# Performance work log

Measured on AMD Instinct MI355X. Metric: run time of the kernel, lower is better.

## Reference

```python
import jax
import jax.numpy as jnp
import numpy as np
from jax import lax

# D dags, L topological levels, K nodes per level, P predecessors per node,
# F = atom/hidden feature dim (104 in original), C = num classes (500)
D, L, K, P, F, C = 256, 64, 64, 8, 104, 500


def setup_inputs() -> dict:
    key = jax.random.key(0)
    ks = jax.random.split(key, 10)
    atom_feats = jax.random.normal(ks[0], (D, L, K, F), dtype=jnp.float32)
    pred_idx = jax.random.randint(ks[1], (D, L - 1, K, P), 0, K, dtype=jnp.int32)
    W1 = jax.random.normal(ks[2], (F, F), dtype=jnp.float32) * 0.1
    b1 = jnp.zeros((F,), dtype=jnp.float32)
    Wm = jax.random.normal(ks[3], (2 * F, F), dtype=jnp.float32) * 0.1
    bm = jnp.zeros((F,), dtype=jnp.float32)
    att_w = jax.random.uniform(ks[4], (F,), dtype=jnp.float32)  # torch.rand init
    dag_w = jax.random.uniform(ks[5], (F,), dtype=jnp.float32)
    Wf = jax.random.normal(ks[6], (F, C), dtype=jnp.float32) * 0.1
    bf = jnp.zeros((C,), dtype=jnp.float32)
    return {"atom_feats": atom_feats, "pred_idx": pred_idx, "W1": W1, "b1": b1,
            "Wm": Wm, "bm": bm, "att_w": att_w, "dag_w": dag_w, "Wf": Wf, "bf": bf}


def reference(atom_feats, pred_idx, W1, b1, Wm, bm, att_w, dag_w, Wf, bf):
    # Level 0: source nodes -> ReLU(NN_single_node(atom))
    out0 = jax.nn.relu(atom_feats[:, 0] @ W1 + b1)  # [D, K, F]

    def step(prev, xs):
        atoms, idx = xs  # atoms [D,K,F], idx [D,K,P]
        # gather predecessor outputs from previous topological level
        preds = jax.vmap(lambda p, i: p[i])(prev, idx)  # [D,K,P,F]
        # softmax attention over the predecessor (stack) axis, elementwise in F
        attn = jax.nn.softmax(att_w * preds, axis=2)
        agg = jnp.sum(attn * preds, axis=2)  # [D,K,F]
        # cat((aggregated, atom)) -> merge -> ReLU
        out = jax.nn.relu(jnp.concatenate([agg, atoms], axis=-1) @ Wm + bm)
        return out, None

    xs = (jnp.swapaxes(atom_feats[:, 1:], 0, 1),  # [L-1, D, K, F]
          jnp.swapaxes(pred_idx, 0, 1))           # [L-1, D, K, P]
    last, _ = lax.scan(step, out0, xs)
    # 'last' output per DAG = last node in topological order
    sink = last[:, -1]  # [D, F]
    # softmax attention over DAG axis with dag_weight, then final linear
    dag_attn = jax.nn.softmax(dag_w * sink, axis=0)
    pooled = jnp.sum(dag_attn * sink, axis=0)  # [F]
    return pooled @ Wf + bf  # [C]
```

## Files before the change

### kernel.cpp

```cpp
#include <hip/hip_runtime.h>
#include <cstddef>
#include <math.h>

#define Dn 256
#define Ln 64
#define Kn 64
#define Pn 8
#define Fn 104
#define Cn 500
#define KF 6656
#define TPB 896
#define PSTR 108
#define XROWB 512
#define NQ 1664

typedef __attribute__((ext_vector_type(8))) short bh8;
typedef __attribute__((ext_vector_type(4))) float f32x4;

__device__ __forceinline__ unsigned short f2bf_rne(float x) {
  unsigned u = __builtin_bit_cast(unsigned, x);
  u = (u + 0x7fffu + ((u >> 16) & 1u)) >> 16;
  return (unsigned short)u;
}
__device__ __forceinline__ float bf2f(unsigned short h) {
  unsigned u = ((unsigned)h) << 16;
  return __builtin_bit_cast(float, u);
}
__device__ __forceinline__ unsigned pkhi(float a, float b) {
  return __builtin_amdgcn_perm(__builtin_bit_cast(unsigned, b),
                               __builtin_bit_cast(unsigned, a), 0x07060302u);
}
__device__ __forceinline__ float hi_of(float x) {
  return __builtin_bit_cast(float, __builtin_bit_cast(unsigned, x) & 0xffff0000u);
}

__device__ __forceinline__ void stage_quad(char* XAc, char* XBc, int k, int c0,
                                           float v0, float v1, float v2, float v3) {
  uint2 hv, lv;
  hv.x = pkhi(v0, v1); hv.y = pkhi(v2, v3);
  const float r0 = v0 - hi_of(v0), r1 = v1 - hi_of(v1);
  const float r2 = v2 - hi_of(v2), r3 = v3 - hi_of(v3);
  lv.x = pkhi(r0, r1); lv.y = pkhi(r2, r3);
  const int off = k * XROWB + ((((c0 >> 3) ^ (k & 7)) << 4) | ((c0 & 7) << 1));
  *reinterpret_cast<uint2*>(XAc + off) = hv;
  *reinterpret_cast<uint2*>(XBc + off) = lv;
}

__device__ __forceinline__ void load_w_frags(const float* __restrict__ Wg, int Krows,
                                             int col, int e, bh8* Wh, bh8* Wl) {
  #pragma unroll
  for (int kt = 0; kt < 7; ++kt) {
    bh8 h, l;
    #pragma unroll
    for (int v = 0; v < 8; ++v) {
      int k = kt * 32 + e * 8 + v;
      float x = (k < Krows && col < Fn) ? Wg[k * Fn + col] : 0.f;
      unsigned short hh = f2bf_rne(x);
      unsigned short ll = f2bf_rne(x - bf2f(hh));
      h[v] = (short)hh; l[v] = (short)ll;
    }
    Wh[kt] = h; Wl[kt] = l;
  }
}

__device__ __forceinline__ void mfma_gemm(const char* XAc, const char* XBc,
                                          const bh8* Wh, const bh8* Wl,
                                          const float* bms, float* PREVs,
                                          int lane, int col, int mh,
                                          int k0, int k1) {
  const int e = lane >> 4;
  const int rb = lane & 15;
  const float bias = (col < Fn) ? bms[col] : 0.f;
  f32x4 acc[2];
  #pragma unroll
  for (int mti = 0; mti < 2; ++mti) { f32x4 b4 = {bias, bias, bias, bias}; acc[mti] = b4; }
  #pragma unroll
  for (int kt = 0; kt < 7; ++kt) {
    if (kt < k0 || kt >= k1) continue;
    #pragma unroll
    for (int mti = 0; mti < 2; ++mti) {
      const int r = (mh * 2 + mti) * 16 + rb;
      const int chunk = (kt * 4 + e) ^ (rb & 7);
      const bh8 ah = *reinterpret_cast<const bh8*>(XAc + r * XROWB + chunk * 16);
      const bh8 al = *reinterpret_cast<const bh8*>(XBc + r * XROWB + chunk * 16);
      acc[mti] = __builtin_amdgcn_mfma_f32_16x16x32_bf16(ah, Wh[kt], acc[mti], 0, 0, 0);
      acc[mti] = __builtin_amdgcn_mfma_f32_16x16x32_bf16(al, Wh[kt], acc[mti], 0, 0, 0);
      acc[mti] = __builtin_amdgcn_mfma_f32_16x16x32_bf16(ah, Wl[kt], acc[mti], 0, 0, 0);
    }
  }
  if (col < Fn) {
    #pragma unroll
    for (int mti = 0; mti < 2; ++mti) {
      #pragma unroll
      for (int j = 0; j < 4; ++j) {
        int r = (mh * 2 + mti) * 16 + e * 4 + j;
        PREVs[r * PSTR + col] = fmaxf(acc[mti][j], 0.f);
      }
    }
  }
}

__global__ __launch_bounds__(TPB) void scan_kernel(
    const float* __restrict__ af,
    const int*   __restrict__ pidx,
    const float* __restrict__ W1, const float* __restrict__ b1,
    const float* __restrict__ Wm, const float* __restrict__ bm,
    const float* __restrict__ att_w,
    float* __restrict__ sink)
{
  extern __shared__ char smem[];
  char*  XAc   = smem;
  char*  XBc   = smem + 32768;
  float* PREVs = (float*)(smem + 65536);
  float* bms   = (float*)(smem + 65536 + 27648);
  float* aws   = (float*)(smem + 65536 + 27648 + 448);
  int*   idxs  = (int*)  (smem + 65536 + 27648 + 448 + 416);

  const int t = threadIdx.x;
  const int d = blockIdx.x;
  const int lane = t & 63;
  const int wvi = t >> 6;
  const int nt = wvi % 7;
  const int mh = wvi / 7;
  const int e = lane >> 4;
  const int col = nt * 16 + (lane & 15);

  const float*  afd = af + (size_t)d * (Ln * KF);
  const float4* af4 = reinterpret_cast<const float4*>(afd);
  const int*    pid = pidx + (size_t)d * ((Ln - 1) * Kn * Pn);

  bh8 Wh[7], Wl[7];
  float4 pf4[2];
  int ir0 = 0;

  for (int i = t; i < 16384; i += TPB) reinterpret_cast<unsigned*>(XAc)[i] = 0u;
  if (t < Fn) { bms[t] = b1[t]; aws[t] = att_w[t]; }
  else if (t < 112) bms[t] = 0.f;
  load_w_frags(W1, Fn, col, e, Wh, Wl);
  #pragma unroll
  for (int j = 0; j < 2; ++j) {
    int q = t + j * TPB;
    if (q < NQ) {
      int k = q / 26, fq = (q - k * 26) << 2;
      float4 v = af4[q];
      stage_quad(XAc, XBc, k, fq, v.x, v.y, v.z, v.w);
    }
  }
  __syncthreads();

  mfma_gemm(XAc, XBc, Wh, Wl, bms, PREVs, lane, col, mh, 0, 4);
  __syncthreads();

  load_w_frags(Wm, 2 * Fn, col, e, Wh, Wl);
  if (t < Fn) bms[t] = bm[t];
  if (t < 512) idxs[t] = pid[t];
  #pragma unroll
  for (int j = 0; j < 2; ++j) {
    int q = t + j * TPB;
    if (q < NQ) pf4[j] = af4[NQ + q];
  }
  __syncthreads();

  for (int l = 1; l < Ln; ++l) {
    #pragma unroll
    for (int j = 0; j < 2; ++j) {
      int q = t + j * TPB;
      if (q < NQ) {
        int k = q / 26, fq = (q - k * 26) << 2;
        float4 v = pf4[j];
        stage_quad(XAc, XBc, k, Fn + fq, v.x, v.y, v.z, v.w);
      }
    }
    if (l < 63) {
      const float4* an = af4 + (size_t)(l + 1) * NQ;
      #pragma unroll
      for (int j = 0; j < 2; ++j) {
        int q = t + j * TPB;
        if (q < NQ) pf4[j] = an[q];
      }
      if (t < 512) ir0 = pid[(size_t)l * 512 + t];
    }
    for (int q = t; q < NQ; q += TPB) {
      int k = q / 26, fq = (q - k * 26) << 2;
      const float4 w4 = *reinterpret_cast<const float4*>(aws + fq);
      const float wa[4] = {w4.x, w4.y, w4.z, w4.w};
      const int4 ia = *reinterpret_cast<const int4*>(idxs + (k << 3));
      const int4 ib = *reinterpret_cast<const int4*>(idxs + (k << 3) + 4);
      const int ip[8] = {ia.x, ia.y, ia.z, ia.w, ib.x, ib.y, ib.z, ib.w};
      float vv[8][4];
      #pragma unroll
      for (int p = 0; p < Pn; ++p) {
        float4 v4 = *reinterpret_cast<const float4*>(PREVs + ip[p] * PSTR + fq);
        vv[p][0] = v4.x; vv[p][1] = v4.y; vv[p][2] = v4.z; vv[p][3] = v4.w;
      }
      float ag[4];
      #pragma unroll
      for (int c = 0; c < 4; ++c) {
        float vmax = fmaxf(fmaxf(fmaxf(fmaxf(fmaxf(fmaxf(fmaxf(
            vv[0][c], vv[1][c]), vv[2][c]), vv[3][c]), vv[4][c]), vv[5][c]), vv[6][c]), vv[7][c]);
        const float m = wa[c] * vmax;
        float es = 0.f, ps = 0.f;
        #pragma unroll
        for (int p = 0; p < Pn; ++p) {
          float ex = __expf(fmaf(wa[c], vv[p][c], -m));
          es += ex; ps += ex * vv[p][c];
        }
        ag[c] = ps * __builtin_amdgcn_rcpf(es);
      }
      stage_quad(XAc, XBc, k, fq, ag[0], ag[1], ag[2], ag[3]);
    }
    __syncthreads();

    mfma_gemm(XAc, XBc, Wh, Wl, bms, PREVs, lane, col, mh, 0, 7);
    if (l < 63 && t < 512) idxs[t] = ir0;
    __syncthreads();
  }

  if (t < Fn) sink[d * Fn + t] = PREVs[(Kn - 1) * PSTR + t];
}

__global__ __launch_bounds__(512) void final_kernel(
    const float* __restrict__ sink, const float* __restrict__ dag_w,
    const float* __restrict__ Wf, const float* __restrict__ bf,
    float* __restrict__ out)
{
  extern __shared__ char smem[];
  float* ss = (float*)smem;
  float* pooled = ss + Dn * Fn;
  const int t = threadIdx.x;
  for (int i = t; i < Dn * Fn; i += 512) ss[i] = sink[i];
  __syncthreads();
  if (t < Fn) {
    float wvv = dag_w[t];
    float m = -3.0e38f;
    for (int dd = 0; dd < Dn; ++dd) m = fmaxf(m, wvv * ss[dd * Fn + t]);
    float es = 0.f, ps = 0.f;
    for (int dd = 0; dd < Dn; ++dd) {
      float v = ss[dd * Fn + t];
      float ex = __expf(wvv * v - m);
      es += ex; ps += ex * v;
    }
    pooled[t] = ps / es;
  }
  __syncthreads();
  if (t < Cn) {
    float a = bf[t];
    for (int f = 0; f < Fn; ++f) a = fmaf(pooled[f], Wf[f * Cn + t], a);
    out[t] = a;
  }
}

extern "C" void kernel_launch(void* const* d_in, const int* in_sizes, int n_in,
                              void* d_out, int out_size, void* d_ws, size_t ws_size,
                              hipStream_t stream) {
  const float* af    = (const float*)d_in[0];
  const int*   pidx  = (const int*)  d_in[1];
  const float* W1    = (const float*)d_in[2];
  const float* b1    = (const float*)d_in[3];
  const float* Wm    = (const float*)d_in[4];
  const float* bm    = (const float*)d_in[5];
  const float* att_w = (const float*)d_in[6];
  const float* dag_w = (const float*)d_in[7];
  const float* Wf    = (const float*)d_in[8];
  const float* bf    = (const float*)d_in[9];
  float* out  = (float*)d_out;
  float* sink = (float*)d_ws;

  constexpr size_t SMEM1 = 96096;
  constexpr size_t SMEM2 = (size_t)(Dn * Fn + Fn) * 4;

  (void)hipFuncSetAttribute((const void*)scan_kernel,
                      hipFuncAttributeMaxDynamicSharedMemorySize, (int)SMEM1);
  (void)hipFuncSetAttribute((const void*)final_kernel,
                      hipFuncAttributeMaxDynamicSharedMemorySize, (int)SMEM2);

  scan_kernel<<<Dn, TPB, SMEM1, stream>>>(af, pidx, W1, b1, Wm, bm, att_w, sink);
  final_kernel<<<1, 512, SMEM2, stream>>>(sink, dag_w, Wf, bf, out);
}
```

Baseline: 354.8 us.

## Split merge GEMM to compute atom-feature half before aggregation

The merge GEMM is split by K-tiles. The atom-feature half (kt 4..6) now runs right after the atom features are staged, before the softmax aggregation. Its partial accumulators are parked in a new shared-memory buffer, and the aggregation half finishes the GEMM after the barrier. This shortens the serial GEMM that follows aggregation and lets MFMA work overlap with the gather phase. The cost is an extra __syncthreads per level, about 28 KB more LDS, and a store/reload of the accumulators.

```diff
diff --git a/kernel.cpp b/kernel.cpp
--- a/kernel.cpp
+++ b/kernel.cpp
@@ -63,31 +63,26 @@
   }
 }
 
-__device__ __forceinline__ void mfma_gemm(const char* XAc, const char* XBc,
-                                          const bh8* Wh, const bh8* Wl,
-                                          const float* bms, float* PREVs,
-                                          int lane, int col, int mh,
-                                          int k0, int k1) {
+__device__ __forceinline__ void mfma_kt(const char* XAc, const char* XBc,
+                                        const bh8* Wh, const bh8* Wl,
+                                        f32x4 acc[2], int kt, int lane, int mh) {
   const int e = lane >> 4;
   const int rb = lane & 15;
-  const float bias = (col < Fn) ? bms[col] : 0.f;
-  f32x4 acc[2];
   #pragma unroll
-  for (int mti = 0; mti < 2; ++mti) { f32x4 b4 = {bias, bias, bias, bias}; acc[mti] = b4; }
-  #pragma unroll
-  for (int kt = 0; kt < 7; ++kt) {
-    if (kt < k0 || kt >= k1) continue;
-    #pragma unroll
-    for (int mti = 0; mti < 2; ++mti) {
-      const int r = (mh * 2 + mti) * 16 + rb;
-      const int chunk = (kt * 4 + e) ^ (rb & 7);
-      const bh8 ah = *reinterpret_cast<const bh8*>(XAc + r * XROWB + chunk * 16);
-      const bh8 al = *reinterpret_cast<const bh8*>(XBc + r * XROWB + chunk * 16);
-      acc[mti] = __builtin_amdgcn_mfma_f32_16x16x32_bf16(ah, Wh[kt], acc[mti], 0, 0, 0);
-      acc[mti] = __builtin_amdgcn_mfma_f32_16x16x32_bf16(al, Wh[kt], acc[mti], 0, 0, 0);
-      acc[mti] = __builtin_amdgcn_mfma_f32_16x16x32_bf16(ah, Wl[kt], acc[mti], 0, 0, 0);
-    }
-  }
+  for (int mti = 0; mti < 2; ++mti) {
+    const int r = (mh * 2 + mti) * 16 + rb;
+    const int chunk = (kt * 4 + e) ^ (rb & 7);
+    const bh8 ah = *reinterpret_cast<const bh8*>(XAc + r * XROWB + chunk * 16);
+    const bh8 al = *reinterpret_cast<const bh8*>(XBc + r * XROWB + chunk * 16);
+    acc[mti] = __builtin_amdgcn_mfma_f32_16x16x32_bf16(ah, Wh[kt], acc[mti], 0, 0, 0);
+    acc[mti] = __builtin_amdgcn_mfma_f32_16x16x32_bf16(al, Wh[kt], acc[mti], 0, 0, 0);
+    acc[mti] = __builtin_amdgcn_mfma_f32_16x16x32_bf16(ah, Wl[kt], acc[mti], 0, 0, 0);
+  }
+}
+
+__device__ __forceinline__ void gemm_epilogue(f32x4 acc[2], float* PREVs,
+                                              int lane, int col, int mh) {
+  const int e = lane >> 4;
   if (col < Fn) {
     #pragma unroll
     for (int mti = 0; mti < 2; ++mti) {
@@ -115,6 +110,7 @@
   float* bms   = (float*)(smem + 65536 + 27648);
   float* aws   = (float*)(smem + 65536 + 27648 + 448);
   int*   idxs  = (int*)  (smem + 65536 + 27648 + 448 + 416);
+  float* PC    = (float*)(smem + 96096);
 
   const int t = threadIdx.x;
   const int d = blockIdx.x;
@@ -148,7 +144,15 @@
   }
   __syncthreads();
 
-  mfma_gemm(XAc, XBc, Wh, Wl, bms, PREVs, lane, col, mh, 0, 4);
+  {
+    const float bias = (col < Fn) ? bms[col] : 0.f;
+    f32x4 acc[2];
+    #pragma unroll
+    for (int mti = 0; mti < 2; ++mti) { f32x4 b4 = {bias, bias, bias, bias}; acc[mti] = b4; }
+    #pragma unroll
+    for (int kt = 0; kt < 4; ++kt) mfma_kt(XAc, XBc, Wh, Wl, acc, kt, lane, mh);
+    gemm_epilogue(acc, PREVs, lane, col, mh);
+  }
   __syncthreads();
 
   load_w_frags(Wm, 2 * Fn, col, e, Wh, Wl);
@@ -171,6 +175,8 @@
         stage_quad(XAc, XBc, k, Fn + fq, v.x, v.y, v.z, v.w);
       }
     }
+    __syncthreads();
+
     if (l < 63) {
       const float4* an = af4 + (size_t)(l + 1) * NQ;
       #pragma unroll
@@ -178,8 +184,20 @@
         int q = t + j * TPB;
         if (q < NQ) pf4[j] = an[q];
       }
-      if (t < 512) ir0 = pid[(size_t)l * 512 + t];
-    }
+      ir0 = (t < 512) ? pid[(size_t)l * 512 + t] : 0;
+    }
+
+    {
+      const float bias = (col < Fn) ? bms[col] : 0.f;
+      f32x4 acc[2];
+      #pragma unroll
+      for (int mti = 0; mti < 2; ++mti) { f32x4 b4 = {bias, bias, bias, bias}; acc[mti] = b4; }
+      #pragma unroll
+      for (int kt = 4; kt < 7; ++kt) mfma_kt(XAc, XBc, Wh, Wl, acc, kt, lane, mh);
+      *reinterpret_cast<f32x4*>(PC + t * 8)     = acc[0];
+      *reinterpret_cast<f32x4*>(PC + t * 8 + 4) = acc[1];
+    }
+
     for (int q = t; q < NQ; q += TPB) {
       int k = q / 26, fq = (q - k * 26) << 2;
       const float4 w4 = *reinterpret_cast<const float4*>(aws + fq);
@@ -211,7 +229,14 @@
     }
     __syncthreads();
 
-    mfma_gemm(XAc, XBc, Wh, Wl, bms, PREVs, lane, col, mh, 0, 7);
+    {
+      f32x4 acc[2];
+      acc[0] = *reinterpret_cast<const f32x4*>(PC + t * 8);
+      acc[1] = *reinterpret_cast<const f32x4*>(PC + t * 8 + 4);
+      #pragma unroll
+      for (int kt = 0; kt < 4; ++kt) mfma_kt(XAc, XBc, Wh, Wl, acc, kt, lane, mh);
+      gemm_epilogue(acc, PREVs, lane, col, mh);
+    }
     if (l < 63 && t < 512) idxs[t] = ir0;
     __syncthreads();
   }
@@ -266,7 +291,7 @@
   float* out  = (float*)d_out;
   float* sink = (float*)d_ws;
 
-  constexpr size_t SMEM1 = 96096;
+  constexpr size_t SMEM1 = 124768;
   constexpr size_t SMEM2 = (size_t)(Dn * Fn + Fn) * 4;
 
   (void)hipFuncSetAttribute((const void*)scan_kernel,
```

New measurement: 376.7 us. +6.2%, slower.
